# Performance work log

Measured on AMD Instinct MI355X. Metric: run time of the kernel, lower is better.

## Reference

```python
import jax, jax.numpy as jnp
import numpy as np

N, E, IN, ED, H, C, G, NC = 50000, 800000, 128, 32, 4, 16, 64, 2
HC = H * C  # 64
NEG_SLOPE = 0.2
EPS = 1e-5


def _layernorm(x, g, b):
    mu = jnp.mean(x, axis=-1, keepdims=True)
    var = jnp.mean((x - mu) ** 2, axis=-1, keepdims=True)
    return (x - mu) * jax.lax.rsqrt(var + EPS) * g + b


def _gat(x, src, dst, edge_attr, W, a_src, a_dst, We, a_edge, b):
    """PyG GATConv (v1) with edge features, concat=True."""
    n = x.shape[0]
    h, c = a_src.shape
    xw = (x @ W).reshape(n, h, c)                       # [N,H,C]
    al_src = jnp.sum(xw * a_src, axis=-1)               # [N,H]
    al_dst = jnp.sum(xw * a_dst, axis=-1)               # [N,H]
    ew = (edge_attr @ We).reshape(-1, h, c)             # [Ef,H,C]
    al_e = jnp.sum(ew * a_edge, axis=-1)                # [Ef,H]
    alpha = al_src[src] + al_dst[dst] + al_e            # [Ef,H]
    alpha = jnp.where(alpha > 0, alpha, NEG_SLOPE * alpha)
    # segment softmax over incoming edges of each dst node
    amax = jax.ops.segment_max(alpha, dst, num_segments=n)
    amax = jnp.where(jnp.isfinite(amax), amax, 0.0)
    ex = jnp.exp(alpha - amax[dst])
    denom = jax.ops.segment_sum(ex, dst, num_segments=n)
    att = ex / (denom[dst] + 1e-16)                     # [Ef,H]
    msg = xw[src] * att[:, :, None]                     # [Ef,H,C]
    out = jax.ops.segment_sum(msg, dst, num_segments=n) # [N,H,C]
    return out.reshape(n, h * c) + b


def setup_inputs() -> dict:
    ks = jax.random.split(jax.random.key(0), 24)
    s = 0.1
    inp = {
        "x": jax.random.normal(ks[0], (N, IN), jnp.float32),
        "edge_attr": jax.random.normal(ks[1], (E, ED), jnp.float32),
        "W1": jax.random.normal(ks[2], (IN, HC), jnp.float32) * s,
        "as1": jax.random.normal(ks[3], (H, C), jnp.float32) * s,
        "ad1": jax.random.normal(ks[4], (H, C), jnp.float32) * s,
        "We1": jax.random.normal(ks[5], (ED, HC), jnp.float32) * s,
        "ae1": jax.random.normal(ks[6], (H, C), jnp.float32) * s,
        "b1": jnp.zeros((HC,), jnp.float32),
        "W2": jax.random.normal(ks[7], (HC, HC), jnp.float32) * s,
        "as2": jax.random.normal(ks[8], (H, C), jnp.float32) * s,
        "ad2": jax.random.normal(ks[9], (H, C), jnp.float32) * s,
        "We2": jax.random.normal(ks[10], (ED, HC), jnp.float32) * s,
        "ae2": jax.random.normal(ks[11], (H, C), jnp.float32) * s,
        "b2": jnp.zeros((HC,), jnp.float32),
        "g1": jnp.ones((HC,), jnp.float32),
        "be1": jnp.zeros((HC,), jnp.float32),
        "fw1": jax.random.normal(ks[12], (HC, 32), jnp.float32) * s,
        "fb1": jnp.zeros((32,), jnp.float32),
        "g2": jnp.ones((32,), jnp.float32),
        "be2": jnp.zeros((32,), jnp.float32),
        "fw2": jax.random.normal(ks[13], (32, NC), jnp.float32) * s,
        "fb2": jnp.zeros((NC,), jnp.float32),
        "edge_index": jax.random.randint(ks[14], (2, E), 0, N, jnp.int64),
        "batch": jnp.sort(jax.random.randint(ks[15], (N,), 0, G, jnp.int64)),
    }
    return inp


def reference(x, edge_attr, W1, as1, ad1, We1, ae1, b1, W2, as2, ad2, We2, ae2,
              b2, g1, be1, fw1, fb1, g2, be2, fw2, fb2, edge_index, batch):
    src, dst = edge_index[0], edge_index[1]
    e = edge_attr.shape[0]
    # add_self_loops with fill_value='mean' (mean of incoming edge_attr per node)
    cnt = jax.ops.segment_sum(jnp.ones((e,), x.dtype), dst, num_segments=N)
    loop_ea = jax.ops.segment_sum(edge_attr, dst, num_segments=N) / jnp.clip(cnt, 1.0)[:, None]
    ar = jnp.arange(N)
    src_f = jnp.concatenate([src, ar])
    dst_f = jnp.concatenate([dst, ar])
    ea_f = jnp.concatenate([edge_attr, loop_ea], axis=0)

    h = _gat(x, src_f, dst_f, ea_f, W1, as1, ad1, We1, ae1, b1)
    h = jax.nn.relu(h)
    h = _layernorm(h, g1, be1)
    h = _gat(h, src_f, dst_f, ea_f, W2, as2, ad2, We2, ae2, b2)
    h = jax.nn.relu(h)
    pooled = jax.ops.segment_max(h, batch, num_segments=G)   # global_max_pool
    pooled = jnp.where(jnp.isfinite(pooled), pooled, 0.0)
    z = pooled @ fw1 + fb1
    z = _layernorm(z, g2, be2)
    z = jax.nn.relu(z)
    # dropout(p=0.4) is identity in eval mode
    z = z @ fw2 + fb2
    return jax.nn.log_softmax(z, axis=1)
```

## Files before the change

### kernel.cpp

```cpp
#include <hip/hip_runtime.h>
#include <math.h>

#define N_NODES 50000
#define N_EDGES 800000
#define IN_DIM 128
#define ED_DIM 32
#define NH 4
#define CH 16
#define HC 64
#define NG 64
#define NCL 2
#define NEG_SLOPE 0.2f
#define LN_EPS 1e-5f
#define NBLK1 196

__global__ void k_ve(const float* __restrict__ We1, const float* __restrict__ ae1,
                     const float* __restrict__ We2, const float* __restrict__ ae2,
                     float* __restrict__ Ve) {
    int t = threadIdx.x;
    int d = t >> 3, k = t & 7;
    int l = k >> 2, h = k & 3;
    const float* We = l ? We2 : We1;
    const float* ae = l ? ae2 : ae1;
    float s = 0.f;
    #pragma unroll
    for (int c = 0; c < CH; ++c) s += We[d * HC + h * CH + c] * ae[h * CH + c];
    Ve[d * 8 + k] = s;
}

__global__ void k_hist(const int* __restrict__ dst, int* __restrict__ cnt) {
    int e = blockIdx.x * 256 + threadIdx.x;
    if (e < N_EDGES) atomicAdd(&cnt[dst[e]], 1);
}

__global__ void k_scan_local(const int* __restrict__ cnt, int* __restrict__ tmp_ex,
                             int* __restrict__ bsum) {
    __shared__ int sd[256];
    int t = threadIdx.x, idx = blockIdx.x * 256 + t;
    int v = (idx < N_NODES) ? cnt[idx] : 0;
    sd[t] = v; __syncthreads();
    for (int off = 1; off < 256; off <<= 1) {
        int add = (t >= off) ? sd[t - off] : 0;
        __syncthreads();
        sd[t] += add;
        __syncthreads();
    }
    if (idx < N_NODES) tmp_ex[idx] = sd[t] - v;
    if (t == 255) bsum[blockIdx.x] = sd[t];
}

__global__ void k_scan_bsums(const int* __restrict__ bsum, int* __restrict__ boff) {
    __shared__ int sd[256];
    int t = threadIdx.x;
    int v = (t < NBLK1) ? bsum[t] : 0;
    sd[t] = v; __syncthreads();
    for (int off = 1; off < 256; off <<= 1) {
        int add = (t >= off) ? sd[t - off] : 0;
        __syncthreads();
        sd[t] += add;
        __syncthreads();
    }
    boff[t] = sd[t] - v;
}

__global__ void k_scan_final(const int* __restrict__ tmp_ex, const int* __restrict__ boff,
                             int* __restrict__ row_start, int* __restrict__ rp) {
    int idx = blockIdx.x * 256 + threadIdx.x;
    if (idx < N_NODES) {
        int v = tmp_ex[idx] + boff[blockIdx.x];
        row_start[idx] = v;
        rp[idx] = v;
    }
    if (idx == 0) row_start[N_NODES] = N_EDGES;
}

__global__ void k_scatter(const int* __restrict__ src, const int* __restrict__ dst,
                          const float* __restrict__ ea, const float* __restrict__ Ve,
                          int* __restrict__ rp,
                          int* __restrict__ src_csr, float* __restrict__ ale_csr) {
    __shared__ float sVe[ED_DIM * 8];
    int t = threadIdx.x;
    if (t < ED_DIM * 8) sVe[t] = Ve[t];
    __syncthreads();
    int e = blockIdx.x * 256 + t;
    if (e >= N_EDGES) return;
    int s = src[e], d = dst[e];
    float a[8];
    #pragma unroll
    for (int k = 0; k < 8; ++k) a[k] = 0.f;
    const float4* er4 = (const float4*)(ea + (long long)e * ED_DIM);
    #pragma unroll
    for (int q = 0; q < ED_DIM / 4; ++q) {
        float4 v = er4[q];
        float ev[4] = {v.x, v.y, v.z, v.w};
        #pragma unroll
        for (int u = 0; u < 4; ++u) {
            #pragma unroll
            for (int k = 0; k < 8; ++k) a[k] += ev[u] * sVe[(q * 4 + u) * 8 + k];
        }
    }
    int pos = atomicAdd(&rp[d], 1);
    src_csr[pos] = s;
    float4* ap = (float4*)(ale_csr + (long long)pos * 8);
    ap[0] = make_float4(a[0], a[1], a[2], a[3]);
    ap[1] = make_float4(a[4], a[5], a[6], a[7]);
}

template<int K>
__global__ void k_xw(const float* __restrict__ X, const float* __restrict__ W,
                     const float* __restrict__ AS, const float* __restrict__ AD,
                     float* __restrict__ XW, float* __restrict__ ALS, float* __restrict__ ALD) {
    __shared__ float sW[K * HC];
    __shared__ float sX[8 * K];
    int t = threadIdx.x;
    for (int i = t; i < K * HC; i += 256) sW[i] = W[i];
    int nb = blockIdx.x * 8;
    for (int i = t; i < 8 * K; i += 256) sX[i] = X[(long long)nb * K + i];
    __syncthreads();
    int sub = t >> 6, j = t & 63;
    const float* x0 = &sX[sub * K];
    const float* x1 = &sX[(sub + 4) * K];
    float acc0 = 0.f, acc1 = 0.f;
    #pragma unroll 8
    for (int k = 0; k < K; ++k) {
        float wv = sW[k * HC + j];
        acc0 += x0[k] * wv;
        acc1 += x1[k] * wv;
    }
    int n0 = nb + sub, n1 = nb + sub + 4;
    XW[(long long)n0 * HC + j] = acc0;
    XW[(long long)n1 * HC + j] = acc1;
    float as_ = AS[j], ad_ = AD[j];
    float vs0 = acc0 * as_, vd0 = acc0 * ad_;
    float vs1 = acc1 * as_, vd1 = acc1 * ad_;
    #pragma unroll
    for (int m = 1; m < 16; m <<= 1) {
        vs0 += __shfl_xor(vs0, m); vd0 += __shfl_xor(vd0, m);
        vs1 += __shfl_xor(vs1, m); vd1 += __shfl_xor(vd1, m);
    }
    if ((j & 15) == 0) {
        int h = j >> 4;
        ALS[n0 * 4 + h] = vs0; ALD[n0 * 4 + h] = vd0;
        ALS[n1 * 4 + h] = vs1; ALD[n1 * 4 + h] = vd1;
    }
}

template<bool DO_LN>
__global__ void k_agg(const int* __restrict__ rs, const int* __restrict__ srcs,
                      const float* __restrict__ ale, int ale_off,
                      const float* __restrict__ ALS, const float* __restrict__ ALD,
                      const float* __restrict__ XW, const float* __restrict__ bias,
                      const float* __restrict__ gam, const float* __restrict__ bet,
                      float* __restrict__ OUT) {
    int n = (blockIdx.x * blockDim.x + threadIdx.x) >> 6;
    if (n >= N_NODES) return;
    int lane = threadIdx.x & 63;
    int h = lane >> 4;
    int e0 = rs[n], e1 = rs[n + 1];
    float adn = ALD[n * 4 + h];
    float acc0 = 0.f, l0 = 0.f, as0 = 0.f;
    float acc1 = 0.f, l1 = 0.f, as1 = 0.f;
    int e = e0;
    for (; e + 1 < e1; e += 2) {
        int sA = srcs[e], sB = srcs[e + 1];
        float aeA = ale[e * 8 + ale_off + h];
        float aeB = ale[(e + 1) * 8 + ale_off + h];
        float xA = XW[sA * HC + lane];
        float xB = XW[sB * HC + lane];
        float aA = ALS[sA * 4 + h] + adn + aeA;
        float aB = ALS[sB * 4 + h] + adn + aeB;
        aA = aA > 0.f ? aA : NEG_SLOPE * aA;
        aB = aB > 0.f ? aB : NEG_SLOPE * aB;
        float pA = __expf(aA), pB = __expf(aB);
        acc0 += pA * xA; l0 += pA; as0 += aeA;
        acc1 += pB * xB; l1 += pB; as1 += aeB;
    }
    if (e < e1) {
        int sA = srcs[e];
        float aeA = ale[e * 8 + ale_off + h];
        float xA = XW[sA * HC + lane];
        float aA = ALS[sA * 4 + h] + adn + aeA;
        aA = aA > 0.f ? aA : NEG_SLOPE * aA;
        float pA = __expf(aA);
        acc0 += pA * xA; l0 += pA; as0 += aeA;
    }
    int d = e1 - e0;
    float invd = 1.f / (float)(d > 0 ? d : 1);
    float aSelf = ALS[n * 4 + h] + adn + (as0 + as1) * invd;
    aSelf = aSelf > 0.f ? aSelf : NEG_SLOPE * aSelf;
    float pS = __expf(aSelf);
    float acc = acc0 + acc1 + pS * XW[n * HC + lane];
    float l = l0 + l1 + pS;
    float v = acc / (l + 1e-16f) + bias[lane];
    v = fmaxf(v, 0.f);
    if (DO_LN) {
        float s1 = v;
        #pragma unroll
        for (int mm = 1; mm < 64; mm <<= 1) s1 += __shfl_xor(s1, mm);
        float mean = s1 * (1.f / 64.f);
        float dd = v - mean;
        float s2 = dd * dd;
        #pragma unroll
        for (int mm = 1; mm < 64; mm <<= 1) s2 += __shfl_xor(s2, mm);
        float var = s2 * (1.f / 64.f);
        v = dd * rsqrtf(var + LN_EPS) * gam[lane] + bet[lane];
    }
    OUT[(long long)n * HC + lane] = v;
}

__global__ void k_pool(const float* __restrict__ H2, const int* __restrict__ batch,
                       float* __restrict__ pooled) {
    int j = threadIdx.x & 63;
    int r = threadIdx.x >> 6;
    int base = blockIdx.x * 128;
    int gcur = -1; float rm = 0.f;
    for (int n = base + r; n < base + 128 && n < N_NODES; n += 4) {
        int g = batch[n];
        if (g != gcur) {
            if (gcur >= 0) atomicMax((unsigned int*)&pooled[gcur * HC + j], __float_as_uint(rm));
            gcur = g; rm = 0.f;
        }
        rm = fmaxf(rm, H2[(long long)n * HC + j]);
    }
    if (gcur >= 0) atomicMax((unsigned int*)&pooled[gcur * HC + j], __float_as_uint(rm));
}

__global__ void k_head(const float* __restrict__ pooled,
                       const float* __restrict__ fw1, const float* __restrict__ fb1,
                       const float* __restrict__ g2, const float* __restrict__ be2,
                       const float* __restrict__ fw2, const float* __restrict__ fb2,
                       float* __restrict__ out) {
    int g = blockIdx.x;
    int j = threadIdx.x;
    float z = 0.f;
    if (j < 32) {
        for (int k = 0; k < HC; ++k) z += pooled[g * HC + k] * fw1[k * 32 + j];
        z += fb1[j];
    }
    float s1 = (j < 32) ? z : 0.f;
    for (int m = 1; m < 32; m <<= 1) s1 += __shfl_xor(s1, m, 32);
    float mean = s1 * (1.f / 32.f);
    float d = z - mean;
    float s2 = (j < 32) ? d * d : 0.f;
    for (int m = 1; m < 32; m <<= 1) s2 += __shfl_xor(s2, m, 32);
    float var = s2 * (1.f / 32.f);
    float zz = 0.f;
    if (j < 32) {
        zz = d * rsqrtf(var + LN_EPS) * g2[j] + be2[j];
        zz = fmaxf(zz, 0.f);
    }
    float p0 = (j < 32) ? zz * fw2[j * NCL + 0] : 0.f;
    float p1 = (j < 32) ? zz * fw2[j * NCL + 1] : 0.f;
    for (int m = 1; m < 32; m <<= 1) { p0 += __shfl_xor(p0, m, 32); p1 += __shfl_xor(p1, m, 32); }
    if (j == 0) {
        float l0 = p0 + fb2[0], l1 = p1 + fb2[1];
        float mx = fmaxf(l0, l1);
        float ls = mx + logf(__expf(l0 - mx) + __expf(l1 - mx));
        out[g * NCL + 0] = l0 - ls;
        out[g * NCL + 1] = l1 - ls;
    }
}

extern "C" void kernel_launch(void* const* d_in, const int* in_sizes, int n_in,
                              void* d_out, int out_size, void* d_ws, size_t ws_size,
                              hipStream_t stream) {
    const float* x   = (const float*)d_in[0];
    const float* ea  = (const float*)d_in[1];
    const float* W1  = (const float*)d_in[2];
    const float* as1 = (const float*)d_in[3];
    const float* ad1 = (const float*)d_in[4];
    const float* We1 = (const float*)d_in[5];
    const float* ae1 = (const float*)d_in[6];
    const float* b1  = (const float*)d_in[7];
    const float* W2  = (const float*)d_in[8];
    const float* as2 = (const float*)d_in[9];
    const float* ad2 = (const float*)d_in[10];
    const float* We2 = (const float*)d_in[11];
    const float* ae2 = (const float*)d_in[12];
    const float* b2  = (const float*)d_in[13];
    const float* g1  = (const float*)d_in[14];
    const float* be1 = (const float*)d_in[15];
    const float* fw1 = (const float*)d_in[16];
    const float* fb1 = (const float*)d_in[17];
    const float* g2  = (const float*)d_in[18];
    const float* be2 = (const float*)d_in[19];
    const float* fw2 = (const float*)d_in[20];
    const float* fb2 = (const float*)d_in[21];
    const int* eidx  = (const int*)d_in[22];
    const int* batch = (const int*)d_in[23];
    const int* srcI = eidx;
    const int* dstI = eidx + N_EDGES;

    char* w = (char*)d_ws;
    auto alloc = [&](size_t bytes) { char* p = w; w += (bytes + 255) & ~(size_t)255; return p; };
    int*   cnt       = (int*)  alloc((size_t)N_NODES * 4);
    int*   row_start = (int*)  alloc((size_t)(N_NODES + 1) * 4);
    int*   rp        = (int*)  alloc((size_t)N_NODES * 4);
    int*   tmp_ex    = (int*)  alloc((size_t)N_NODES * 4);
    int*   bsum      = (int*)  alloc(256 * 4);
    int*   boff      = (int*)  alloc(256 * 4);
    float* Ve        = (float*)alloc(ED_DIM * 8 * 4);
    int*   src_csr   = (int*)  alloc((size_t)N_EDGES * 4);
    float* ale_csr   = (float*)alloc((size_t)N_EDGES * 8 * 4);
    float* xw1       = (float*)alloc((size_t)N_NODES * HC * 4);
    float* als1      = (float*)alloc((size_t)N_NODES * 4 * 4);
    float* ald1      = (float*)alloc((size_t)N_NODES * 4 * 4);
    float* h1        = (float*)alloc((size_t)N_NODES * HC * 4);
    float* als2      = (float*)alloc((size_t)N_NODES * 4 * 4);
    float* ald2      = (float*)alloc((size_t)N_NODES * 4 * 4);
    float* pooled    = (float*)alloc((size_t)NG * HC * 4);
    float* xw2 = xw1;
    float* h2  = h1;

    hipMemsetAsync(cnt, 0, (size_t)N_NODES * 4, stream);
    hipMemsetAsync(pooled, 0, (size_t)NG * HC * 4, stream);

    k_ve<<<1, 256, 0, stream>>>(We1, ae1, We2, ae2, Ve);
    k_hist<<<N_EDGES / 256, 256, 0, stream>>>(dstI, cnt);
    k_scan_local<<<NBLK1, 256, 0, stream>>>(cnt, tmp_ex, bsum);
    k_scan_bsums<<<1, 256, 0, stream>>>(bsum, boff);
    k_scan_final<<<NBLK1, 256, 0, stream>>>(tmp_ex, boff, row_start, rp);
    k_scatter<<<N_EDGES / 256, 256, 0, stream>>>(srcI, dstI, ea, Ve, rp, src_csr, ale_csr);

    k_xw<IN_DIM><<<N_NODES / 8, 256, 0, stream>>>(x, W1, as1, ad1, xw1, als1, ald1);
    k_agg<true><<<N_NODES / 4, 256, 0, stream>>>(row_start, src_csr, ale_csr, 0,
                                                 als1, ald1, xw1, b1, g1, be1, h1);
    k_xw<HC><<<N_NODES / 8, 256, 0, stream>>>(h1, W2, as2, ad2, xw2, als2, ald2);
    k_agg<false><<<N_NODES / 4, 256, 0, stream>>>(row_start, src_csr, ale_csr, 4,
                                                  als2, ald2, xw2, b2, nullptr, nullptr, h2);

    k_pool<<<(N_NODES + 127) / 128, 256, 0, stream>>>(h2, batch, pooled);
    k_head<<<NG, 64, 0, stream>>>(pooled, fw1, fb1, g2, be2, fw2, fb2, (float*)d_out);
}
```

Before: 495.2 us.

## Store edge logits in edge order, index via packed CSR; unroll aggregation by four

The edge kernel now writes per-edge attention logits contiguously in original edge order and scatters only a packed (src, edge id) pair into CSR order. This replaces the scattered 32-byte ale writes with coalesced ones. The aggregation kernel reads the pair and gathers ale through the edge id, which adds a random gather per edge in both layers. The aggregation loop is also unrolled from two to four independent accumulators to expose more memory-level parallelism.

```diff
diff --git a/kernel.cpp b/kernel.cpp
--- a/kernel.cpp
+++ b/kernel.cpp
@@ -74,17 +74,16 @@
     if (idx == 0) row_start[N_NODES] = N_EDGES;
 }
 
-__global__ void k_scatter(const int* __restrict__ src, const int* __restrict__ dst,
-                          const float* __restrict__ ea, const float* __restrict__ Ve,
-                          int* __restrict__ rp,
-                          int* __restrict__ src_csr, float* __restrict__ ale_csr) {
+__global__ void k_edge(const int* __restrict__ src, const int* __restrict__ dst,
+                       const float* __restrict__ ea, const float* __restrict__ Ve,
+                       int* __restrict__ rp,
+                       int2* __restrict__ pk_csr, float* __restrict__ ale_edge) {
     __shared__ float sVe[ED_DIM * 8];
     int t = threadIdx.x;
     if (t < ED_DIM * 8) sVe[t] = Ve[t];
     __syncthreads();
     int e = blockIdx.x * 256 + t;
     if (e >= N_EDGES) return;
-    int s = src[e], d = dst[e];
     float a[8];
     #pragma unroll
     for (int k = 0; k < 8; ++k) a[k] = 0.f;
@@ -99,11 +98,12 @@
             for (int k = 0; k < 8; ++k) a[k] += ev[u] * sVe[(q * 4 + u) * 8 + k];
         }
     }
-    int pos = atomicAdd(&rp[d], 1);
-    src_csr[pos] = s;
-    float4* ap = (float4*)(ale_csr + (long long)pos * 8);
+    float4* ap = (float4*)(ale_edge + (long long)e * 8);
     ap[0] = make_float4(a[0], a[1], a[2], a[3]);
     ap[1] = make_float4(a[4], a[5], a[6], a[7]);
+    int d = dst[e];
+    int pos = atomicAdd(&rp[d], 1);
+    pk_csr[pos] = make_int2(src[e], e);
 }
 
 template<int K>
@@ -146,7 +146,7 @@
 }
 
 template<bool DO_LN>
-__global__ void k_agg(const int* __restrict__ rs, const int* __restrict__ srcs,
+__global__ void k_agg(const int* __restrict__ rs, const int2* __restrict__ pk,
                       const float* __restrict__ ale, int ale_off,
                       const float* __restrict__ ALS, const float* __restrict__ ALD,
                       const float* __restrict__ XW, const float* __restrict__ bias,
@@ -160,37 +160,49 @@
     float adn = ALD[n * 4 + h];
     float acc0 = 0.f, l0 = 0.f, as0 = 0.f;
     float acc1 = 0.f, l1 = 0.f, as1 = 0.f;
+    float acc2 = 0.f, l2 = 0.f, as2 = 0.f;
+    float acc3 = 0.f, l3 = 0.f, as3 = 0.f;
     int e = e0;
-    for (; e + 1 < e1; e += 2) {
-        int sA = srcs[e], sB = srcs[e + 1];
-        float aeA = ale[e * 8 + ale_off + h];
-        float aeB = ale[(e + 1) * 8 + ale_off + h];
-        float xA = XW[sA * HC + lane];
-        float xB = XW[sB * HC + lane];
-        float aA = ALS[sA * 4 + h] + adn + aeA;
-        float aB = ALS[sB * 4 + h] + adn + aeB;
+    for (; e + 3 < e1; e += 4) {
+        int2 pA = pk[e], pB = pk[e + 1], pC = pk[e + 2], pD = pk[e + 3];
+        float aeA = ale[(long long)pA.y * 8 + ale_off + h];
+        float aeB = ale[(long long)pB.y * 8 + ale_off + h];
+        float aeC = ale[(long long)pC.y * 8 + ale_off + h];
+        float aeD = ale[(long long)pD.y * 8 + ale_off + h];
+        float xA = XW[pA.x * HC + lane];
+        float xB = XW[pB.x * HC + lane];
+        float xC = XW[pC.x * HC + lane];
+        float xD = XW[pD.x * HC + lane];
+        float aA = ALS[pA.x * 4 + h] + adn + aeA;
+        float aB = ALS[pB.x * 4 + h] + adn + aeB;
+        float aC = ALS[pC.x * 4 + h] + adn + aeC;
+        float aD = ALS[pD.x * 4 + h] + adn + aeD;
         aA = aA > 0.f ? aA : NEG_SLOPE * aA;
         aB = aB > 0.f ? aB : NEG_SLOPE * aB;
-        float pA = __expf(aA), pB = __expf(aB);
-        acc0 += pA * xA; l0 += pA; as0 += aeA;
-        acc1 += pB * xB; l1 += pB; as1 += aeB;
-    }
-    if (e < e1) {
-        int sA = srcs[e];
-        float aeA = ale[e * 8 + ale_off + h];
-        float xA = XW[sA * HC + lane];
-        float aA = ALS[sA * 4 + h] + adn + aeA;
+        aC = aC > 0.f ? aC : NEG_SLOPE * aC;
+        aD = aD > 0.f ? aD : NEG_SLOPE * aD;
+        float qA = __expf(aA), qB = __expf(aB), qC = __expf(aC), qD = __expf(aD);
+        acc0 += qA * xA; l0 += qA; as0 += aeA;
+        acc1 += qB * xB; l1 += qB; as1 += aeB;
+        acc2 += qC * xC; l2 += qC; as2 += aeC;
+        acc3 += qD * xD; l3 += qD; as3 += aeD;
+    }
+    for (; e < e1; ++e) {
+        int2 pA = pk[e];
+        float aeA = ale[(long long)pA.y * 8 + ale_off + h];
+        float xA = XW[pA.x * HC + lane];
+        float aA = ALS[pA.x * 4 + h] + adn + aeA;
         aA = aA > 0.f ? aA : NEG_SLOPE * aA;
-        float pA = __expf(aA);
-        acc0 += pA * xA; l0 += pA; as0 += aeA;
+        float qA = __expf(aA);
+        acc0 += qA * xA; l0 += qA; as0 += aeA;
     }
     int d = e1 - e0;
     float invd = 1.f / (float)(d > 0 ? d : 1);
-    float aSelf = ALS[n * 4 + h] + adn + (as0 + as1) * invd;
+    float aSelf = ALS[n * 4 + h] + adn + (as0 + as1 + as2 + as3) * invd;
     aSelf = aSelf > 0.f ? aSelf : NEG_SLOPE * aSelf;
     float pS = __expf(aSelf);
-    float acc = acc0 + acc1 + pS * XW[n * HC + lane];
-    float l = l0 + l1 + pS;
+    float acc = (acc0 + acc1) + (acc2 + acc3) + pS * XW[n * HC + lane];
+    float l = (l0 + l1) + (l2 + l3) + pS;
     float v = acc / (l + 1e-16f) + bias[lane];
     v = fmaxf(v, 0.f);
     if (DO_LN) {
@@ -300,8 +312,8 @@
     int*   bsum      = (int*)  alloc(256 * 4);
     int*   boff      = (int*)  alloc(256 * 4);
     float* Ve        = (float*)alloc(ED_DIM * 8 * 4);
-    int*   src_csr   = (int*)  alloc((size_t)N_EDGES * 4);
-    float* ale_csr   = (float*)alloc((size_t)N_EDGES * 8 * 4);
+    int2*  pk_csr    = (int2*) alloc((size_t)N_EDGES * 8);
+    float* ale_edge  = (float*)alloc((size_t)N_EDGES * 8 * 4);
     float* xw1       = (float*)alloc((size_t)N_NODES * HC * 4);
     float* als1      = (float*)alloc((size_t)N_NODES * 4 * 4);
     float* ald1      = (float*)alloc((size_t)N_NODES * 4 * 4);
@@ -320,13 +332,13 @@
     k_scan_local<<<NBLK1, 256, 0, stream>>>(cnt, tmp_ex, bsum);
     k_scan_bsums<<<1, 256, 0, stream>>>(bsum, boff);
     k_scan_final<<<NBLK1, 256, 0, stream>>>(tmp_ex, boff, row_start, rp);
-    k_scatter<<<N_EDGES / 256, 256, 0, stream>>>(srcI, dstI, ea, Ve, rp, src_csr, ale_csr);
+    k_edge<<<N_EDGES / 256, 256, 0, stream>>>(srcI, dstI, ea, Ve, rp, pk_csr, ale_edge);
 
     k_xw<IN_DIM><<<N_NODES / 8, 256, 0, stream>>>(x, W1, as1, ad1, xw1, als1, ald1);
-    k_agg<true><<<N_NODES / 4, 256, 0, stream>>>(row_start, src_csr, ale_csr, 0,
+    k_agg<true><<<N_NODES / 4, 256, 0, stream>>>(row_start, pk_csr, ale_edge, 0,
                                                  als1, ald1, xw1, b1, g1, be1, h1);
     k_xw<HC><<<N_NODES / 8, 256, 0, stream>>>(h1, W2, as2, ad2, xw2, als2, ald2);
-    k_agg<false><<<N_NODES / 4, 256, 0, stream>>>(row_start, src_csr, ale_csr, 4,
+    k_agg<false><<<N_NODES / 4, 256, 0, stream>>>(row_start, pk_csr, ale_edge, 4,
                                                   als2, ald2, xw2, b2, nullptr, nullptr, h2);
 
     k_pool<<<(N_NODES + 127) / 128, 256, 0, stream>>>(h2, batch, pooled);
```

New measurement: 483.9 us. 1.02x faster.
